# Kernel optimization log

Measured on AMD Instinct MI355X. Metric: run time of the kernel, lower is better.

## Reference

```python
import jax, jax.numpy as jnp
import numpy as np

V = 10000
E = 60000
B = 8
LATENT = 512
HIDDEN = 256
NUM_LAYERS = 5


def setup_inputs() -> dict:
    key = jax.random.key(0)
    ks = jax.random.split(key, 12)
    vertex_xyz = jax.random.normal(ks[0], (V, 3), dtype=jnp.float32)
    latent = jax.random.normal(ks[1], (B, LATENT), dtype=jnp.float32)
    edge_index = jax.random.randint(ks[2], (2, E), 0, V, dtype=jnp.int64)
    s = 0.02
    input_W = jax.random.normal(ks[3], (HIDDEN, LATENT + 3), dtype=jnp.float32) * s
    input_b = jnp.zeros((HIDDEN,), dtype=jnp.float32)
    conv_W = jax.random.normal(ks[4], (NUM_LAYERS, HIDDEN, HIDDEN), dtype=jnp.float32) * s
    conv_b = jnp.zeros((NUM_LAYERS, HIDDEN), dtype=jnp.float32)
    out_W = jax.random.normal(ks[5], (3, HIDDEN), dtype=jnp.float32) * s
    out_b = jnp.zeros((3,), dtype=jnp.float32)
    return dict(vertex_xyz=vertex_xyz, latent=latent, edge_index=edge_index,
                input_W=input_W, input_b=input_b, conv_W=conv_W, conv_b=conv_b,
                out_W=out_W, out_b=out_b)


def _gcn_norm(edge_index, num_nodes):
    # PyG GCNConv default: add self-loops, symmetric normalization.
    src, dst = edge_index[0], edge_index[1]
    loop = jnp.arange(num_nodes, dtype=src.dtype)
    src = jnp.concatenate([src, loop])
    dst = jnp.concatenate([dst, loop])
    deg = jax.ops.segment_sum(jnp.ones_like(dst, dtype=jnp.float32), dst,
                              num_segments=num_nodes)
    dinv = jnp.where(deg > 0, jax.lax.rsqrt(deg), 0.0)
    norm = dinv[src] * dinv[dst]  # [E+V]
    return src, dst, norm


def reference(vertex_xyz, latent, edge_index, input_W, input_b, conv_W, conv_b, out_W, out_b):
    Bn, Vn = latent.shape[0], vertex_xyz.shape[0]
    # Build node features: concat template xyz with broadcast latent -> [B, V, 3+latent]
    x = jnp.concatenate([
        jnp.broadcast_to(vertex_xyz[None], (Bn, Vn, 3)),
        jnp.broadcast_to(latent[:, None, :], (Bn, Vn, latent.shape[1])),
    ], axis=-1)
    x = jax.nn.relu(jnp.einsum('bvf,hf->bvh', x, input_W) + input_b)

    # The batched edge_index is a per-graph copy offset by b*V, so normalization
    # and message passing are identical per batch; vectorize over B.
    src, dst, norm = _gcn_norm(edge_index, Vn)
    for l in range(conv_W.shape[0]):
        h = jnp.einsum('bvh,oh->bvo', x, conv_W[l])        # linear transform
        msg = h[:, src, :] * norm[None, :, None]           # gather + scale
        agg = jnp.zeros_like(h).at[:, dst, :].add(msg)     # scatter-add
        x = jax.nn.relu(agg + conv_b[l])

    disp = jnp.einsum('bvh,oh->bvo', x, out_W) + out_b     # [B, V, 3]
    return disp
```

## Files before the change

kernel.cpp:

```cpp
#include <hip/hip_runtime.h>

#define Vn 10000
#define En 60000
#define Bb 8
#define LAT 512
#define HID 256
#define NL 5
#define Mrows (Bb * Vn)

typedef __attribute__((ext_vector_type(4))) int    i32x4;
typedef __attribute__((ext_vector_type(4))) float  f32x4;
typedef __attribute__((ext_vector_type(8))) short  bf16x8;
typedef __attribute__((ext_vector_type(4))) unsigned short u16x4;

__device__ __forceinline__ float bf2f(unsigned short u) {
    union { unsigned int u; float f; } c;
    c.u = ((unsigned int)u) << 16;
    return c.f;
}
__device__ __forceinline__ unsigned short f2bf(float f) {
    union { float f; unsigned int u; } c;
    c.f = f;
    unsigned int u = c.u + 0x7FFFu + ((c.u >> 16) & 1u);
    return (unsigned short)(u >> 16);
}


__global__ void k_init(int* cnt, int* cur) {
    int i = blockIdx.x * blockDim.x + threadIdx.x;
    if (i < Vn) { cnt[i] = 0; cur[i] = 0; }
}

__global__ void k_count(const int* __restrict__ dst, int* __restrict__ cnt) {
    int e = blockIdx.x * blockDim.x + threadIdx.x;
    if (e < En) atomicAdd(&cnt[dst[e]], 1);
}

__global__ void k_dinv(const int* __restrict__ cnt, float* __restrict__ dinv,
                       float* __restrict__ selfn) {
    int v = blockIdx.x * blockDim.x + threadIdx.x;
    if (v < Vn) {
        float d = (float)cnt[v] + 1.0f;
        float r = rsqrtf(d);
        dinv[v] = r;
        selfn[v] = r * r;
    }
}

__global__ void k_scan(const int* __restrict__ cnt, int* __restrict__ rowptr) {
    __shared__ int part[1024];
    const int PER = 10;
    int tid = threadIdx.x;
    int base = tid * PER;
    int local[PER];
    int s = 0;
#pragma unroll
    for (int i = 0; i < PER; ++i) {
        int idx = base + i;
        int c = (idx < Vn) ? cnt[idx] : 0;
        local[i] = s;
        s += c;
    }
    part[tid] = s;
    __syncthreads();
    for (int off = 1; off < 1024; off <<= 1) {
        int add = (tid >= off) ? part[tid - off] : 0;
        __syncthreads();
        part[tid] += add;
        __syncthreads();
    }
    int chunk_base = part[tid] - s;
#pragma unroll
    for (int i = 0; i < PER; ++i) {
        int idx = base + i;
        if (idx < Vn) rowptr[idx] = chunk_base + local[i];
    }
    if (tid == 1023) rowptr[Vn] = part[1023];
}

__global__ void k_fill(const int* __restrict__ src, const int* __restrict__ dst,
                       const float* __restrict__ dinv, const int* __restrict__ rowptr,
                       int* __restrict__ cur, int* __restrict__ csr_src,
                       float* __restrict__ csr_norm) {
    int e = blockIdx.x * blockDim.x + threadIdx.x;
    if (e < En) {
        int s = src[e], d = dst[e];
        int p = atomicAdd(&cur[d], 1);
        int idx = rowptr[d] + p;
        csr_src[idx] = s;
        csr_norm[idx] = dinv[s] * dinv[d];
    }
}


__global__ void k_wcvt(const float* __restrict__ W, unsigned short* __restrict__ Wb, int n) {
    int i = blockIdx.x * blockDim.x + threadIdx.x;
    if (i < n) Wb[i] = f2bf(W[i]);
}


__global__ void k_latc(const float* __restrict__ latent, const float* __restrict__ input_W,
                       const float* __restrict__ input_b, float* __restrict__ latc) {
    int i = blockIdx.x * blockDim.x + threadIdx.x;
    if (i < Bb * HID) {
        int b = i / HID, h = i % HID;
        const float* w = input_W + (size_t)h * (LAT + 3) + 3;
        const float* l = latent + (size_t)b * LAT;
        float s = input_b[h];
        for (int k = 0; k < LAT; ++k) s = fmaf(l[k], w[k], s);
        latc[i] = s;
    }
}

__global__ __launch_bounds__(256) void k_input(const float* __restrict__ xyz,
                                               const float* __restrict__ input_W,
                                               const float* __restrict__ latc,
                                               unsigned short* __restrict__ X) {
    int bv = blockIdx.x;
    int h = threadIdx.x;
    int v = bv % Vn;
    int b = bv / Vn;
    const float* w = input_W + (size_t)h * (LAT + 3);
    float x0 = xyz[v * 3 + 0], x1 = xyz[v * 3 + 1], x2 = xyz[v * 3 + 2];
    float s = latc[b * HID + h];
    s = fmaf(x0, w[0], s);
    s = fmaf(x1, w[1], s);
    s = fmaf(x2, w[2], s);
    X[(size_t)bv * HID + h] = f2bf(fmaxf(s, 0.0f));
}


__global__ __launch_bounds__(256) void k_agg(const unsigned short* __restrict__ Xin,
                                             unsigned short* __restrict__ Xa,
                                             const int* __restrict__ rowptr,
                                             const int* __restrict__ csr_src,
                                             const float* __restrict__ csr_norm,
                                             const float* __restrict__ selfn) {
    int wid = threadIdx.x >> 6;
    int lane = threadIdx.x & 63;
    int bv = blockIdx.x * 4 + wid;
    int b = bv / Vn;
    int v = bv - b * Vn;
    int f = lane << 2;
    size_t bbase = (size_t)b * Vn * HID;

    u16x4 hs = *(const u16x4*)&Xin[(size_t)bv * HID + f];
    float sn = selfn[v];
    float a0 = sn * bf2f(hs[0]), a1 = sn * bf2f(hs[1]);
    float a2 = sn * bf2f(hs[2]), a3 = sn * bf2f(hs[3]);

    int s = rowptr[v], e = rowptr[v + 1];
    int i = s;
    for (; i + 2 <= e; i += 2) {
        float n0 = csr_norm[i], n1 = csr_norm[i + 1];
        int s0 = csr_src[i], s1 = csr_src[i + 1];
        u16x4 h0 = *(const u16x4*)&Xin[bbase + (size_t)s0 * HID + f];
        u16x4 h1 = *(const u16x4*)&Xin[bbase + (size_t)s1 * HID + f];
        a0 = fmaf(n0, bf2f(h0[0]), a0); a1 = fmaf(n0, bf2f(h0[1]), a1);
        a2 = fmaf(n0, bf2f(h0[2]), a2); a3 = fmaf(n0, bf2f(h0[3]), a3);
        a0 = fmaf(n1, bf2f(h1[0]), a0); a1 = fmaf(n1, bf2f(h1[1]), a1);
        a2 = fmaf(n1, bf2f(h1[2]), a2); a3 = fmaf(n1, bf2f(h1[3]), a3);
    }
    if (i < e) {
        float n0 = csr_norm[i];
        u16x4 h0 = *(const u16x4*)&Xin[bbase + (size_t)csr_src[i] * HID + f];
        a0 = fmaf(n0, bf2f(h0[0]), a0); a1 = fmaf(n0, bf2f(h0[1]), a1);
        a2 = fmaf(n0, bf2f(h0[2]), a2); a3 = fmaf(n0, bf2f(h0[3]), a3);
    }
    u16x4 r;
    r[0] = f2bf(a0); r[1] = f2bf(a1); r[2] = f2bf(a2); r[3] = f2bf(a3);
    *(u16x4*)&Xa[(size_t)bv * HID + f] = r;
}


__global__ __launch_bounds__(256) void k_gemm(const unsigned short* __restrict__ A,
                                              const unsigned short* __restrict__ Wb,
                                              const float* __restrict__ bias,
                                              unsigned short* __restrict__ Xout) {
    __shared__ __align__(16) char smem[32768];
    const int t = threadIdx.x;
    const int w = t >> 6;
    const int l = t & 63;
    const int m0 = blockIdx.x * 64;
    const int n0w = w * 64;
    const int lr = l & 15;
    const int lg = l >> 4;

    bf16x8 Bf[4][8];
#pragma unroll
    for (int nt = 0; nt < 4; ++nt) {
        const unsigned short* wp = Wb + (size_t)(n0w + nt * 16 + lr) * HID + lg * 8;
#pragma unroll
        for (int ks = 0; ks < 8; ++ks)
            Bf[nt][ks] = __builtin_bit_cast(bf16x8, *(const i32x4*)(wp + ks * 32));
    }

    {
        const char* src = (const char*)(A + (size_t)m0 * HID);
#pragma unroll
        for (int i = 0; i < 8; ++i) {
            int x = i * 4096 + t * 16;
            i32x4 v = *(const i32x4*)(src + x);
            int sw = (x & ~511) | ((x & 511) ^ (((x >> 9) & 7) << 4));
            *(i32x4*)(smem + sw) = v;
        }
    }
    __syncthreads();

    f32x4 acc[4][4];
#pragma unroll
    for (int mt = 0; mt < 4; ++mt)
#pragma unroll
        for (int nt = 0; nt < 4; ++nt)
            acc[mt][nt] = (f32x4){0.f, 0.f, 0.f, 0.f};

#pragma unroll
    for (int ks = 0; ks < 8; ++ks) {
#pragma unroll
        for (int mt = 0; mt < 4; ++mt) {
            int row = mt * 16 + lr;
            int colb = ks * 64 + lg * 16;
            int addr = row * 512 + (colb ^ ((row & 7) << 4));
            bf16x8 a = __builtin_bit_cast(bf16x8, *(const i32x4*)(smem + addr));
#pragma unroll
            for (int nt = 0; nt < 4; ++nt)
                acc[mt][nt] = __builtin_amdgcn_mfma_f32_16x16x32_bf16(
                    a, Bf[nt][ks], acc[mt][nt], 0, 0, 0);
        }
    }

    __syncthreads();

    float bnt[4];
#pragma unroll
    for (int nt = 0; nt < 4; ++nt) bnt[nt] = bias[n0w + nt * 16 + lr];

#pragma unroll
    for (int mt = 0; mt < 4; ++mt)
#pragma unroll
        for (int nt = 0; nt < 4; ++nt)
#pragma unroll
            for (int r = 0; r < 4; ++r) {
                int row = mt * 16 + lg * 4 + r;
                int col = n0w + nt * 16 + lr;
                float vv = fmaxf(acc[mt][nt][r] + bnt[nt], 0.0f);
                int addr = row * 512 + (((col * 2) & 511) ^ ((row & 7) << 4));
                *(unsigned short*)(smem + addr) = f2bf(vv);
            }
    __syncthreads();

    char* dstb = (char*)(Xout + (size_t)m0 * HID);
#pragma unroll
    for (int i = 0; i < 8; ++i) {
        int x = i * 4096 + t * 16;
        int sw = (x & ~511) | ((x & 511) ^ (((x >> 9) & 7) << 4));
        *(i32x4*)(dstb + x) = *(const i32x4*)(smem + sw);
    }
}


__global__ __launch_bounds__(256) void k_out(const unsigned short* __restrict__ X,
                                             const float* __restrict__ oW,
                                             const float* __restrict__ ob,
                                             float* __restrict__ disp) {
    int wid = threadIdx.x >> 6;
    int lane = threadIdx.x & 63;
    int bv = blockIdx.x * 4 + wid;
    int f = lane << 2;
    u16x4 xv = *(const u16x4*)&X[(size_t)bv * HID + f];
    float x0 = bf2f(xv[0]), x1 = bf2f(xv[1]), x2 = bf2f(xv[2]), x3 = bf2f(xv[3]);
    float p[3];
#pragma unroll
    for (int c = 0; c < 3; ++c) {
        f32x4 wv = *(const f32x4*)&oW[c * HID + f];
        p[c] = x0 * wv[0] + x1 * wv[1] + x2 * wv[2] + x3 * wv[3];
    }
#pragma unroll
    for (int off = 32; off > 0; off >>= 1) {
#pragma unroll
        for (int c = 0; c < 3; ++c) p[c] += __shfl_down(p[c], off, 64);
    }
    if (lane == 0) {
#pragma unroll
        for (int c = 0; c < 3; ++c) disp[(size_t)bv * 3 + c] = p[c] + ob[c];
    }
}


extern "C" void kernel_launch(void* const* d_in, const int* in_sizes, int n_in,
                              void* d_out, int out_size, void* d_ws, size_t ws_size,
                              hipStream_t stream) {
    const float* xyz     = (const float*)d_in[0];
    const float* latent  = (const float*)d_in[1];
    const int*   eidx    = (const int*)d_in[2];
    const float* input_W = (const float*)d_in[3];
    const float* input_b = (const float*)d_in[4];
    const float* conv_W  = (const float*)d_in[5];
    const float* conv_b  = (const float*)d_in[6];
    const float* out_W   = (const float*)d_in[7];
    const float* out_b   = (const float*)d_in[8];
    float* disp = (float*)d_out;

    const int* src = eidx;
    const int* dst = eidx + En;

    char* base = (char*)d_ws;
    size_t off = 0;
    auto alloc = [&](size_t bytes) {
        size_t o = off;
        off = (off + bytes + 255) & ~(size_t)255;
        return (void*)(base + o);
    };
    int*   cnt      = (int*)alloc(Vn * 4);
    int*   cur      = (int*)alloc(Vn * 4);
    float* dinv     = (float*)alloc(Vn * 4);
    float* selfn    = (float*)alloc(Vn * 4);
    int*   rowptr   = (int*)alloc((Vn + 1) * 4);
    int*   csr_src  = (int*)alloc(En * 4);
    float* csr_norm = (float*)alloc(En * 4);
    float* latc     = (float*)alloc(Bb * HID * 4);
    unsigned short* Wb = (unsigned short*)alloc((size_t)NL * HID * HID * 2);
    unsigned short* X  = (unsigned short*)alloc((size_t)Mrows * HID * 2);
    unsigned short* Xa = (unsigned short*)alloc((size_t)Mrows * HID * 2);

    k_init<<<(Vn + 255) / 256, 256, 0, stream>>>(cnt, cur);
    k_count<<<(En + 255) / 256, 256, 0, stream>>>(dst, cnt);
    k_dinv<<<(Vn + 255) / 256, 256, 0, stream>>>(cnt, dinv, selfn);
    k_scan<<<1, 1024, 0, stream>>>(cnt, rowptr);
    k_fill<<<(En + 255) / 256, 256, 0, stream>>>(src, dst, dinv, rowptr, cur, csr_src, csr_norm);

    k_wcvt<<<(NL * HID * HID + 255) / 256, 256, 0, stream>>>(conv_W, Wb, NL * HID * HID);

    k_latc<<<(Bb * HID + 255) / 256, 256, 0, stream>>>(latent, input_W, input_b, latc);
    k_input<<<Mrows, 256, 0, stream>>>(xyz, input_W, latc, X);

    for (int l = 0; l < NL; ++l) {
        k_agg<<<Mrows / 4, 256, 0, stream>>>(X, Xa, rowptr, csr_src, csr_norm, selfn);
        k_gemm<<<Mrows / 64, 256, 0, stream>>>(Xa, Wb + (size_t)l * HID * HID,
                                               conv_b + (size_t)l * HID, X);
    }

    k_out<<<Mrows / 4, 256, 0, stream>>>(X, out_W, out_b, disp);
}
```

Measured before the change: 553.1 us.

## Fuse GCN aggregation into GEMM tile load and ping-pong feature buffers

The sparse neighbour aggregation is now computed directly into the GEMM's shared-memory A tile, so each layer becomes one kernel. This drops the separate aggregation kernel and the write and re-read of the aggregated feature matrix through global memory. Each GEMM block now performs gathers serially over 16 rows per wave before any MFMA work starts, which may lower latency hiding compared with the many small aggregation blocks used before. The input-layer kernels are also restructured: the latent dot product is split across 4 lanes with a shuffle reduction, and the xyz weights are pre-transposed so each thread writes 8 outputs.

```diff
diff --git a/kernel.cpp b/kernel.cpp
--- a/kernel.cpp
+++ b/kernel.cpp
@@ -99,84 +99,61 @@
 }
 
 
-__global__ void k_latc(const float* __restrict__ latent, const float* __restrict__ input_W,
-                       const float* __restrict__ input_b, float* __restrict__ latc) {
-    int i = blockIdx.x * blockDim.x + threadIdx.x;
-    if (i < Bb * HID) {
-        int b = i / HID, h = i % HID;
-        const float* w = input_W + (size_t)h * (LAT + 3) + 3;
-        const float* l = latent + (size_t)b * LAT;
-        float s = input_b[h];
-        for (int k = 0; k < LAT; ++k) s = fmaf(l[k], w[k], s);
-        latc[i] = s;
-    }
+__global__ __launch_bounds__(256) void k_latc(const float* __restrict__ latent,
+                                              const float* __restrict__ input_W,
+                                              const float* __restrict__ input_b,
+                                              float* __restrict__ latc,
+                                              float* __restrict__ w3p) {
+    int gid = blockIdx.x * 256 + threadIdx.x;
+    int q = gid & 3;
+    int i = gid >> 2;
+    int b = i >> 8, h = i & 255;
+    const float* wr = input_W + (size_t)h * (LAT + 3) + 3 + q * 128;
+    const float* lr = latent + (size_t)b * LAT + q * 128;
+    float s = 0.0f;
+#pragma unroll 8
+    for (int k = 0; k < 128; ++k) s = fmaf(lr[k], wr[k], s);
+    s += __shfl_xor(s, 1, 64);
+    s += __shfl_xor(s, 2, 64);
+    if (q == 0) latc[i] = s + input_b[h];
+    if (gid < 768) w3p[gid] = input_W[(size_t)(gid & 255) * (LAT + 3) + (gid >> 8)];
 }
 
 __global__ __launch_bounds__(256) void k_input(const float* __restrict__ xyz,
-                                               const float* __restrict__ input_W,
+                                               const float* __restrict__ w3p,
                                                const float* __restrict__ latc,
                                                unsigned short* __restrict__ X) {
-    int bv = blockIdx.x;
-    int h = threadIdx.x;
-    int v = bv % Vn;
-    int b = bv / Vn;
-    const float* w = input_W + (size_t)h * (LAT + 3);
+    int gid = blockIdx.x * 256 + threadIdx.x;
+    int row = gid >> 5;
+    int hc = (gid & 31) << 3;
+    int b = row / Vn;
+    int v = row - b * Vn;
     float x0 = xyz[v * 3 + 0], x1 = xyz[v * 3 + 1], x2 = xyz[v * 3 + 2];
-    float s = latc[b * HID + h];
-    s = fmaf(x0, w[0], s);
-    s = fmaf(x1, w[1], s);
-    s = fmaf(x2, w[2], s);
-    X[(size_t)bv * HID + h] = f2bf(fmaxf(s, 0.0f));
-}
-
-
-__global__ __launch_bounds__(256) void k_agg(const unsigned short* __restrict__ Xin,
-                                             unsigned short* __restrict__ Xa,
-                                             const int* __restrict__ rowptr,
-                                             const int* __restrict__ csr_src,
-                                             const float* __restrict__ csr_norm,
-                                             const float* __restrict__ selfn) {
-    int wid = threadIdx.x >> 6;
-    int lane = threadIdx.x & 63;
-    int bv = blockIdx.x * 4 + wid;
-    int b = bv / Vn;
-    int v = bv - b * Vn;
-    int f = lane << 2;
-    size_t bbase = (size_t)b * Vn * HID;
-
-    u16x4 hs = *(const u16x4*)&Xin[(size_t)bv * HID + f];
-    float sn = selfn[v];
-    float a0 = sn * bf2f(hs[0]), a1 = sn * bf2f(hs[1]);
-    float a2 = sn * bf2f(hs[2]), a3 = sn * bf2f(hs[3]);
-
-    int s = rowptr[v], e = rowptr[v + 1];
-    int i = s;
-    for (; i + 2 <= e; i += 2) {
-        float n0 = csr_norm[i], n1 = csr_norm[i + 1];
-        int s0 = csr_src[i], s1 = csr_src[i + 1];
-        u16x4 h0 = *(const u16x4*)&Xin[bbase + (size_t)s0 * HID + f];
-        u16x4 h1 = *(const u16x4*)&Xin[bbase + (size_t)s1 * HID + f];
-        a0 = fmaf(n0, bf2f(h0[0]), a0); a1 = fmaf(n0, bf2f(h0[1]), a1);
-        a2 = fmaf(n0, bf2f(h0[2]), a2); a3 = fmaf(n0, bf2f(h0[3]), a3);
-        a0 = fmaf(n1, bf2f(h1[0]), a0); a1 = fmaf(n1, bf2f(h1[1]), a1);
-        a2 = fmaf(n1, bf2f(h1[2]), a2); a3 = fmaf(n1, bf2f(h1[3]), a3);
-    }
-    if (i < e) {
-        float n0 = csr_norm[i];
-        u16x4 h0 = *(const u16x4*)&Xin[bbase + (size_t)csr_src[i] * HID + f];
-        a0 = fmaf(n0, bf2f(h0[0]), a0); a1 = fmaf(n0, bf2f(h0[1]), a1);
-        a2 = fmaf(n0, bf2f(h0[2]), a2); a3 = fmaf(n0, bf2f(h0[3]), a3);
-    }
-    u16x4 r;
-    r[0] = f2bf(a0); r[1] = f2bf(a1); r[2] = f2bf(a2); r[3] = f2bf(a3);
-    *(u16x4*)&Xa[(size_t)bv * HID + f] = r;
-}
-
-
-__global__ __launch_bounds__(256) void k_gemm(const unsigned short* __restrict__ A,
-                                              const unsigned short* __restrict__ Wb,
-                                              const float* __restrict__ bias,
-                                              unsigned short* __restrict__ Xout) {
+    const float* lc = latc + b * HID + hc;
+    u16x4 o0, o1;
+#pragma unroll
+    for (int j = 0; j < 8; ++j) {
+        float s = lc[j];
+        s = fmaf(x0, w3p[hc + j], s);
+        s = fmaf(x1, w3p[256 + hc + j], s);
+        s = fmaf(x2, w3p[512 + hc + j], s);
+        unsigned short r = f2bf(fmaxf(s, 0.0f));
+        if (j < 4) o0[j] = r; else o1[j - 4] = r;
+    }
+    u16x4* dst = (u16x4*)&X[(size_t)row * HID + hc];
+    dst[0] = o0;
+    dst[1] = o1;
+}
+
+
+__global__ __launch_bounds__(256) void k_fused(const unsigned short* __restrict__ Xin,
+                                               const unsigned short* __restrict__ Wb,
+                                               const float* __restrict__ bias,
+                                               const int* __restrict__ rowptr,
+                                               const int* __restrict__ csr_src,
+                                               const float* __restrict__ csr_norm,
+                                               const float* __restrict__ selfn,
+                                               unsigned short* __restrict__ Xout) {
     __shared__ __align__(16) char smem[32768];
     const int t = threadIdx.x;
     const int w = t >> 6;
@@ -196,13 +173,42 @@
     }
 
     {
-        const char* src = (const char*)(A + (size_t)m0 * HID);
-#pragma unroll
-        for (int i = 0; i < 8; ++i) {
-            int x = i * 4096 + t * 16;
-            i32x4 v = *(const i32x4*)(src + x);
-            int sw = (x & ~511) | ((x & 511) ^ (((x >> 9) & 7) << 4));
-            *(i32x4*)(smem + sw) = v;
+        const int f = l << 2;
+        for (int rr = 0; rr < 16; ++rr) {
+            const int r = w * 16 + rr;
+            const int row = m0 + r;
+            const int b = row / Vn;
+            const int v = row - b * Vn;
+            const size_t bbase = (size_t)b * Vn * HID;
+
+            u16x4 hs = *(const u16x4*)&Xin[(size_t)row * HID + f];
+            float sn = selfn[v];
+            float a0 = sn * bf2f(hs[0]), a1 = sn * bf2f(hs[1]);
+            float a2 = sn * bf2f(hs[2]), a3 = sn * bf2f(hs[3]);
+
+            int s = rowptr[v], e = rowptr[v + 1];
+            int i = s;
+            for (; i + 2 <= e; i += 2) {
+                float n0 = csr_norm[i], n1 = csr_norm[i + 1];
+                int s0 = csr_src[i], s1 = csr_src[i + 1];
+                u16x4 h0 = *(const u16x4*)&Xin[bbase + (size_t)s0 * HID + f];
+                u16x4 h1 = *(const u16x4*)&Xin[bbase + (size_t)s1 * HID + f];
+                a0 = fmaf(n0, bf2f(h0[0]), a0); a1 = fmaf(n0, bf2f(h0[1]), a1);
+                a2 = fmaf(n0, bf2f(h0[2]), a2); a3 = fmaf(n0, bf2f(h0[3]), a3);
+                a0 = fmaf(n1, bf2f(h1[0]), a0); a1 = fmaf(n1, bf2f(h1[1]), a1);
+                a2 = fmaf(n1, bf2f(h1[2]), a2); a3 = fmaf(n1, bf2f(h1[3]), a3);
+            }
+            if (i < e) {
+                float n0 = csr_norm[i];
+                u16x4 h0 = *(const u16x4*)&Xin[bbase + (size_t)csr_src[i] * HID + f];
+                a0 = fmaf(n0, bf2f(h0[0]), a0); a1 = fmaf(n0, bf2f(h0[1]), a1);
+                a2 = fmaf(n0, bf2f(h0[2]), a2); a3 = fmaf(n0, bf2f(h0[3]), a3);
+            }
+            u16x4 ov;
+            ov[0] = f2bf(a0); ov[1] = f2bf(a1); ov[2] = f2bf(a2); ov[3] = f2bf(a3);
+            int boff = f * 2;
+            int addr = r * 512 + (boff ^ ((r & 7) << 4));
+            *(u16x4*)(smem + addr) = ov;
         }
     }
     __syncthreads();
@@ -319,6 +325,7 @@
     int*   csr_src  = (int*)alloc(En * 4);
     float* csr_norm = (float*)alloc(En * 4);
     float* latc     = (float*)alloc(Bb * HID * 4);
+    float* w3p      = (float*)alloc(3 * HID * 4);
     unsigned short* Wb = (unsigned short*)alloc((size_t)NL * HID * HID * 2);
     unsigned short* X  = (unsigned short*)alloc((size_t)Mrows * HID * 2);
     unsigned short* Xa = (unsigned short*)alloc((size_t)Mrows * HID * 2);
@@ -331,14 +338,17 @@
 
     k_wcvt<<<(NL * HID * HID + 255) / 256, 256, 0, stream>>>(conv_W, Wb, NL * HID * HID);
 
-    k_latc<<<(Bb * HID + 255) / 256, 256, 0, stream>>>(latent, input_W, input_b, latc);
-    k_input<<<Mrows, 256, 0, stream>>>(xyz, input_W, latc, X);
-
+    k_latc<<<32, 256, 0, stream>>>(latent, input_W, input_b, latc, w3p);
+    k_input<<<Mrows * 32 / 256, 256, 0, stream>>>(xyz, w3p, latc, X);
+
+    unsigned short* ping = X;
+    unsigned short* pong = Xa;
     for (int l = 0; l < NL; ++l) {
-        k_agg<<<Mrows / 4, 256, 0, stream>>>(X, Xa, rowptr, csr_src, csr_norm, selfn);
-        k_gemm<<<Mrows / 64, 256, 0, stream>>>(Xa, Wb + (size_t)l * HID * HID,
-                                               conv_b + (size_t)l * HID, X);
-    }
-
-    k_out<<<Mrows / 4, 256, 0, stream>>>(X, out_W, out_b, disp);
-}
+        k_fused<<<Mrows / 64, 256, 0, stream>>>(ping, Wb + (size_t)l * HID * HID,
+                                                conv_b + (size_t)l * HID,
+                                                rowptr, csr_src, csr_norm, selfn, pong);
+        unsigned short* tmp = ping; ping = pong; pong = tmp;
+    }
+
+    k_out<<<Mrows / 4, 256, 0, stream>>>(ping, out_W, out_b, disp);
+}
```

Result: slower. 1.175 ms (+112.5%).
